# Performance work log

Hardware: AMD Instinct MI355X
Metric: run time of the kernel (lower is better)

Reference implementation:

```python
import jax, jax.numpy as jnp
import numpy as np

N = 100000   # nodes of target type
N1 = 80000   # nodes of second type
D = 128      # raw feature dim
H = 64       # hidden dim
C = 16       # n_classes
G = 3        # number of graphs (metapaths)
E = 1000000  # edges per graph
K = 20       # neighbors per node for NS branch
LP_LAYERS = 3


def setup_inputs() -> dict:
    key = jax.random.key(0)
    ks = jax.random.split(key, 24)
    f = lambda i, shape: jax.random.normal(ks[i], shape, dtype=jnp.float32)
    feats0 = f(0, (N, D))
    feats1 = f(1, (N1, D))
    W0 = f(2, (D, H)) * 0.05
    b0 = jnp.zeros((H,), jnp.float32)
    W1 = f(3, (D, H)) * 0.05
    b1 = jnp.zeros((H,), jnp.float32)
    Wp = f(4, (D, H)) * 0.05
    Wcls = f(5, (H, C)) * 0.05
    bcls = jnp.zeros((C,), jnp.float32)
    alpha = f(6, (N, 1)) * 0.1
    attention = f(7, (N, G, 1))
    y = jax.random.randint(ks[8], (N,), 0, C)
    labels_one_hot = jax.nn.one_hot(y, C, dtype=jnp.float32)
    byte_idx_train = jax.random.bernoulli(ks[9], 0.3, (N, 1))
    label_init = jnp.full((N, C), 1.0 / C, jnp.float32)
    nei_idx = jax.random.randint(ks[10], (N, K), 0, N1, dtype=jnp.int32)
    src0 = jax.random.randint(ks[11], (E,), 0, N, dtype=jnp.int32)
    dst0 = jax.random.randint(ks[12], (E,), 0, N, dtype=jnp.int32)
    src1 = jax.random.randint(ks[13], (E,), 0, N, dtype=jnp.int32)
    dst1 = jax.random.randint(ks[14], (E,), 0, N, dtype=jnp.int32)
    src2 = jax.random.randint(ks[15], (E,), 0, N, dtype=jnp.int32)
    dst2 = jax.random.randint(ks[16], (E,), 0, N, dtype=jnp.int32)
    return dict(feats0=feats0, feats1=feats1, W0=W0, b0=b0, W1=W1, b1=b1,
                Wp=Wp, Wcls=Wcls, bcls=bcls, alpha=alpha, attention=attention,
                labels_one_hot=labels_one_hot, label_init=label_init,
                byte_idx_train=byte_idx_train, nei_idx=nei_idx,
                src0=src0, dst0=dst0, src1=src1, dst1=dst1, src2=src2, dst2=dst2)


def _propagate(fp, h, src, dst, n):
    # edge attention: dot-product score of projected feats, softmax per dst
    s = jnp.sum(fp[src] * fp[dst], axis=-1) / np.sqrt(fp.shape[-1])   # [E]
    m = jax.ops.segment_max(s, dst, num_segments=n)                   # [N]
    e = jnp.exp(s - jnp.where(jnp.isfinite(m), m, 0.0)[dst])          # [E]
    denom = jax.ops.segment_sum(e, dst, num_segments=n)               # [N]
    att = e / (denom[dst] + 1e-16)                                    # [E]
    return jax.ops.segment_sum(att[:, None] * h[src], dst, num_segments=n)


def reference(feats0, feats1, W0, b0, W1, b1, Wp, Wcls, bcls, alpha, attention,
              labels_one_hot, label_init, byte_idx_train, nei_idx,
              src0, dst0, src1, dst1, src2, dst2):
    n = label_init.shape[0]
    masked = byte_idx_train.astype(jnp.float32)          # [N,1]
    masked_label = 1.0 - masked                          # (~mask).float()
    masked_onehot = labels_one_hot * masked              # clamp train labels

    fp = feats0 @ Wp                                     # shared projected feats [N,H]
    h_prime = []
    for src, dst in ((src0, dst0), (src1, dst1), (src2, dst2)):
        h = label_init
        for _ in range(LP_LAYERS):
            h = _propagate(fp, h, src, dst, n)
            h = h * masked_label + masked_onehot
        h_prime.append(h)
    x = jnp.stack(h_prime, axis=-1)                      # [N, C, G]
    att_g = jax.nn.softmax(attention, axis=1)            # [N, G, 1]
    logits_lp = jnp.matmul(x, att_g).squeeze(-1)         # [N, C]

    # NS_ec branch: per-type projection + neighbor-mean aggregation + classifier
    h0 = feats0 @ W0 + b0                                # [N, H]
    h1 = feats1 @ W1 + b1                                # [N1, H]
    z = h0 + jnp.mean(h1[nei_idx], axis=1)               # [N, H]
    logits_ns = z @ Wcls + bcls                          # [N, C]

    gate = jax.nn.sigmoid(alpha)
    logits = gate * logits_lp + jax.nn.sigmoid(-alpha) * logits_ns
    return logits, logits_lp, logits_ns
```

## Files before the change

### kernel.cpp

```cpp
#include <hip/hip_runtime.h>
#include <stdint.h>
#include <stddef.h>

__device__ __forceinline__ float bl(unsigned u){ return __uint_as_float(u << 16); }
__device__ __forceinline__ float bh(unsigned u){ return __uint_as_float(u & 0xffff0000u); }
__device__ __forceinline__ unsigned short f2bf(float f){
    unsigned u = __float_as_uint(f);
    unsigned r = (u + 0x7fffu + ((u >> 16) & 1u)) >> 16;
    return (unsigned short)r;
}
__device__ __forceinline__ void ntstore_u2(uint2* p, unsigned x, unsigned y){
    unsigned long long v = ((unsigned long long)y << 32) | (unsigned long long)x;
    __builtin_nontemporal_store(v, (unsigned long long*)p);
}
__device__ __forceinline__ float get_mask(const void* p, unsigned flags, int i){
    if((flags & 1u) == 0) return ((const int*)p)[i] ? 1.0f : 0.0f;
    if(flags & 2u)        return ((const float*)p)[i];
    return ((const unsigned char*)p)[i] ? 1.0f : 0.0f;
}

__global__ __launch_bounds__(256) void prep_kernel(
    const float* __restrict__ W0, const float* __restrict__ b0,
    const float* __restrict__ W1, const float* __restrict__ b1,
    const float* __restrict__ Wcls, const float* __restrict__ bcls,
    float* __restrict__ W0c, float* __restrict__ W1c,
    float* __restrict__ b0c, float* __restrict__ b1c,
    const unsigned char* __restrict__ mp, int n,
    const unsigned* __restrict__ li, long li_n, unsigned* __restrict__ flags)
{
    int t = threadIdx.x;
    if(blockIdx.x == 0){
        for(int i = t; i < 2048; i += 256){
            int d = i >> 4, c = i & 15;
            float s0 = 0.f, s1 = 0.f;
            for(int k = 0; k < 64; k++){
                float wc = Wcls[k*16 + c];
                s0 += W0[d*64 + k]*wc;
                s1 += W1[d*64 + k]*wc;
            }
            W0c[i] = s0; W1c[i] = s1;
        }
        if(t < 16){
            float s0 = 0.f, s1 = 0.f;
            for(int k = 0; k < 64; k++){
                float wc = Wcls[k*16 + t];
                s0 += b0[k]*wc; s1 += b1[k]*wc;
            }
            b0c[t] = s0 + bcls[t];
            b1c[t] = s1;
        }
    } else {
        long i = (long)(blockIdx.x - 1)*256 + t;
        unsigned f = 0;
        if(i < n){
            unsigned char b = mp[i];
            if((i & 3) && b) f |= 1u;
            if(b == 0x3Fu)   f |= 2u;
        }
        if(i < li_n){
            if(li[i] != li[0]) f |= 4u;
        }
        if(f) atomicOr(flags, f);
    }
}

__global__ __launch_bounds__(256) void proj_fused0(
    const float* __restrict__ X, const float* __restrict__ Wp,
    const float* __restrict__ W0c, const float* __restrict__ b0c,
    unsigned short* __restrict__ fph, float* __restrict__ h0c, int rows)
{
    __shared__ float Wl[128*64];
    __shared__ float Wcl[128*16];
    __shared__ float ftile[32*128];
    int t = threadIdx.x;
    for(int i = t; i < 2048; i += 256) ((float4*)Wl)[i]  = ((const float4*)Wp)[i];
    for(int i = t; i < 512;  i += 256) ((float4*)Wcl)[i] = ((const float4*)W0c)[i];
    int c4 = (t & 15)*4;
    int col16 = t & 15;
    int r2 = (t >> 4)*2;
    float bc = b0c[col16];
    for(long base = (long)blockIdx.x*32; base < rows; base += (long)gridDim.x*32){
        int nr = min(32, (int)(rows - base));
        __syncthreads();
        for(int i = t; i < nr*32; i += 256){
            int r = i >> 5, q = i & 31;
            ((float4*)ftile)[r*32 + q] = ((const float4*)X)[(base + r)*32 + q];
        }
        __syncthreads();
        float a00=0,a01=0,a02=0,a03=0, a10=0,a11=0,a12=0,a13=0;
        float c0 = bc, c1 = bc;
        #pragma unroll 4
        for(int k = 0; k < 128; k++){
            float4 w = *((const float4*)(Wl + k*64 + c4));
            float wc = Wcl[k*16 + col16];
            float x0 = ftile[r2*128 + k];
            float x1 = ftile[(r2+1)*128 + k];
            a00 += x0*w.x; a01 += x0*w.y; a02 += x0*w.z; a03 += x0*w.w; c0 += x0*wc;
            a10 += x1*w.x; a11 += x1*w.y; a12 += x1*w.z; a13 += x1*w.w; c1 += x1*wc;
        }
        if(r2 < nr){
            ushort4 o; o.x=f2bf(a00); o.y=f2bf(a01); o.z=f2bf(a02); o.w=f2bf(a03);
            *((ushort4*)(fph + (base + r2)*64 + c4)) = o;
            h0c[(base + r2)*16 + col16] = c0;
        }
        if(r2 + 1 < nr){
            ushort4 o; o.x=f2bf(a10); o.y=f2bf(a11); o.z=f2bf(a12); o.w=f2bf(a13);
            *((ushort4*)(fph + (base + r2 + 1)*64 + c4)) = o;
            h0c[(base + r2 + 1)*16 + col16] = c1;
        }
    }
}

__global__ __launch_bounds__(256) void proj16_count_kernel(
    const float* __restrict__ X, const float* __restrict__ Wc,
    const float* __restrict__ biasc, unsigned short* __restrict__ Y, int rows,
    int nbProj,
    const int* __restrict__ dst0, const int* __restrict__ dst1, const int* __restrict__ dst2,
    int* __restrict__ deg, int n, int eg)
{
    __shared__ float Wcl[128*16];
    __shared__ float ftile[64*128];
    int t = threadIdx.x;
    if(blockIdx.x < nbProj){
        for(int i = t; i < 512; i += 256) ((float4*)Wcl)[i] = ((const float4*)Wc)[i];
        int col = t & 15;
        int r4 = (t >> 4)*4;
        float bc = biasc[col];
        long base = (long)blockIdx.x*64;
        if(base < rows){
            int nr = min(64, (int)(rows - base));
            __syncthreads();
            for(int i = t; i < nr*32; i += 256){
                int r = i >> 5, q = i & 31;
                ((float4*)ftile)[r*32 + q] = ((const float4*)X)[(base + r)*32 + q];
            }
            __syncthreads();
            float acc0 = bc, acc1 = bc, acc2 = bc, acc3 = bc;
            #pragma unroll 4
            for(int k = 0; k < 128; k++){
                float wc = Wcl[k*16 + col];
                acc0 += ftile[(r4+0)*128 + k]*wc;
                acc1 += ftile[(r4+1)*128 + k]*wc;
                acc2 += ftile[(r4+2)*128 + k]*wc;
                acc3 += ftile[(r4+3)*128 + k]*wc;
            }
            if(r4+0 < nr) Y[(base + r4 + 0)*16 + col] = f2bf(acc0);
            if(r4+1 < nr) Y[(base + r4 + 1)*16 + col] = f2bf(acc1);
            if(r4+2 < nr) Y[(base + r4 + 2)*16 + col] = f2bf(acc2);
            if(r4+3 < nr) Y[(base + r4 + 3)*16 + col] = f2bf(acc3);
        }
    } else {
        long tid = (long)(blockIdx.x - nbProj)*256 + t;
        if(tid < 3L*eg){
            int g = (int)(tid / eg);
            int e = (int)(tid - (long)g*eg);
            const int* dp = g==0 ? dst0 : (g==1 ? dst1 : dst2);
            atomicAdd(&deg[(long)g*n + dp[e]], 1);
        }
    }
}

__global__ __launch_bounds__(256) void scanA_kernel(const int* __restrict__ deg,
                                                    int* __restrict__ incl,
                                                    int* __restrict__ bsum, int n3)
{
    __shared__ int sh[256];
    int t = threadIdx.x;
    long base = (long)blockIdx.x*1024 + t*4;
    int v0=0,v1=0,v2=0,v3=0;
    if(base   < n3) v0 = deg[base];
    if(base+1 < n3) v1 = deg[base+1];
    if(base+2 < n3) v2 = deg[base+2];
    if(base+3 < n3) v3 = deg[base+3];
    int tot = v0+v1+v2+v3;
    sh[t] = tot;
    __syncthreads();
    for(int ofs = 1; ofs < 256; ofs <<= 1){
        int add = (t >= ofs) ? sh[t-ofs] : 0;
        __syncthreads();
        sh[t] += add;
        __syncthreads();
    }
    int pre = sh[t] - tot;
    if(t == 255) bsum[blockIdx.x] = sh[255];
    int s0 = pre+v0, s1 = s0+v1, s2 = s1+v2, s3 = s2+v3;
    if(base   < n3) incl[base]   = s0;
    if(base+1 < n3) incl[base+1] = s1;
    if(base+2 < n3) incl[base+2] = s2;
    if(base+3 < n3) incl[base+3] = s3;
}

__global__ __launch_bounds__(512) void scanB_kernel(int* __restrict__ bsum, int nb)
{
    __shared__ int sh[512];
    int t = threadIdx.x;
    int v = (t < nb) ? bsum[t] : 0;
    sh[t] = v;
    __syncthreads();
    for(int ofs = 1; ofs < 512; ofs <<= 1){
        int add = (t >= ofs) ? sh[t-ofs] : 0;
        __syncthreads();
        sh[t] += add;
        __syncthreads();
    }
    if(t < nb) bsum[t] = sh[t] - v;
}

__global__ __launch_bounds__(256) void scanC_kernel(const int* __restrict__ incl,
                                                    const int* __restrict__ boff,
                                                    int* __restrict__ rowptr,
                                                    int* __restrict__ cursor, int n3)
{
    int i = blockIdx.x*blockDim.x + threadIdx.x;
    if(i >= n3) return;
    int ex = (i == 0) ? 0 : (incl[i-1] + boff[(i-1) >> 10]);
    rowptr[i] = ex;
    cursor[i] = ex;
    if(i == n3-1) rowptr[n3] = incl[i] + boff[i >> 10];
}

__global__ __launch_bounds__(256) void score_scatter_packed(
    const unsigned short* __restrict__ fph,
    const int* __restrict__ src0, const int* __restrict__ dst0,
    const int* __restrict__ src1, const int* __restrict__ dst1,
    const int* __restrict__ src2, const int* __restrict__ dst2,
    int* __restrict__ cursor, uint2* __restrict__ rec, int n, int eg)
{
    long tid = (long)blockIdx.x*blockDim.x + threadIdx.x;
    long gid = tid >> 3;
    long tot = 3L*eg;
    long e0 = gid*4;
    if(e0 >= tot) return;
    int l = threadIdx.x & 7;
    const uint4* f4 = (const uint4*)fph;

    int sv[4], dv[4], gv[4];
    bool ok[4];
    #pragma unroll
    for(int q = 0; q < 4; q++){
        long e = e0 + q;
        ok[q] = (e < tot);
        long ee = ok[q] ? e : (tot - 1);
        int g = (int)(ee / eg);
        int i = (int)(ee - (long)g*eg);
        const int* sp = g==0 ? src0 : (g==1 ? src1 : src2);
        const int* dp = g==0 ? dst0 : (g==1 ? dst1 : dst2);
        sv[q] = sp[i];
        dv[q] = dp[i];
        gv[q] = g;
    }
    uint4 A[4], B[4];
    #pragma unroll
    for(int q = 0; q < 4; q++){
        A[q] = f4[(long)sv[q]*8 + l];
        B[q] = f4[(long)dv[q]*8 + l];
    }
    float p[4];
    #pragma unroll
    for(int q = 0; q < 4; q++){
        float v;
        v  = bl(A[q].x)*bl(B[q].x) + bh(A[q].x)*bh(B[q].x);
        v += bl(A[q].y)*bl(B[q].y) + bh(A[q].y)*bh(B[q].y);
        v += bl(A[q].z)*bl(B[q].z) + bh(A[q].z)*bh(B[q].z);
        v += bl(A[q].w)*bl(B[q].w) + bh(A[q].w)*bh(B[q].w);
        p[q] = v;
    }
    #pragma unroll
    for(int q = 0; q < 4; q++){
        p[q] += __shfl_xor(p[q], 1);
        p[q] += __shfl_xor(p[q], 2);
        p[q] += __shfl_xor(p[q], 4);
    }
    if(l == 0){
        int pos[4];
        #pragma unroll
        for(int q = 0; q < 4; q++){
            if(ok[q]) pos[q] = atomicAdd(&cursor[(long)gv[q]*n + dv[q]], 1);
        }
        #pragma unroll
        for(int q = 0; q < 4; q++){
            if(ok[q]){
                float ev = __expf(fminf(p[q]*0.125f, 70.0f));
                ntstore_u2(&rec[pos[q]], (unsigned)sv[q], __float_as_uint(ev));
            }
        }
    }
}

__device__ __forceinline__ void prop_row_bf16(
    const uint2* __restrict__ rec, int beg, int end,
    const unsigned short* __restrict__ hg, int c4,
    float &a0, float &a1, float &a2, float &a3)
{
    float den = 0.f;
    a0 = a1 = a2 = a3 = 0.f;
    int j = beg;
    if((j & 1) && j < end){
        uint2 r = rec[j];
        float e = __uint_as_float(r.y);
        den += e;
        uint2 hv = *((const uint2*)(hg + (long)r.x*16 + c4));
        a0 += e*bl(hv.x); a1 += e*bh(hv.x); a2 += e*bl(hv.y); a3 += e*bh(hv.y);
        j++;
    }
    for(; j + 1 < end; j += 2){
        uint4 rr = *((const uint4*)(&rec[j]));
        float e0 = __uint_as_float(rr.y);
        float e1 = __uint_as_float(rr.w);
        den += e0 + e1;
        uint2 hv0 = *((const uint2*)(hg + (long)rr.x*16 + c4));
        uint2 hv1 = *((const uint2*)(hg + (long)rr.z*16 + c4));
        a0 += e0*bl(hv0.x) + e1*bl(hv1.x);
        a1 += e0*bh(hv0.x) + e1*bh(hv1.x);
        a2 += e0*bl(hv0.y) + e1*bl(hv1.y);
        a3 += e0*bh(hv0.y) + e1*bh(hv1.y);
    }
    if(j < end){
        uint2 r = rec[j];
        float e = __uint_as_float(r.y);
        den += e;
        uint2 hv = *((const uint2*)(hg + (long)r.x*16 + c4));
        a0 += e*bl(hv.x); a1 += e*bh(hv.x); a2 += e*bl(hv.y); a3 += e*bh(hv.y);
    }
    float inv = 1.0f/(den + 1e-16f);
    a0 *= inv; a1 *= inv; a2 *= inv; a3 *= inv;
}

template<int L1>
__global__ __launch_bounds__(256) void propagate_rec_kernel(
    const int* __restrict__ rowptr, const uint2* __restrict__ rec,
    const float* __restrict__ h_in_f32, const unsigned short* __restrict__ h_in_bf,
    unsigned short* __restrict__ h_next, const float* __restrict__ labels,
    const void* __restrict__ maskp, const unsigned* __restrict__ flags, int n)
{
    long tid = (long)blockIdx.x*blockDim.x + threadIdx.x;
    int row = (int)(tid >> 2);
    int c4 = (int)(tid & 3)*4;
    if(row >= 3*n) return;
    int g = row / n;
    int d = row - g*n;
    int beg = rowptr[row], end = rowptr[row+1];
    unsigned fl = *flags;
    float a0=0.f, a1=0.f, a2=0.f, a3=0.f;
    if(L1 && !(fl & 4u)){
        float v = (end > beg) ? h_in_f32[0] : 0.f;
        a0 = a1 = a2 = a3 = v;
    } else if(L1){
        float den = 0.f;
        for(int j = beg; j < end; j++){
            uint2 r = rec[j];
            float e = __uint_as_float(r.y);
            den += e;
            float4 hv = *((const float4*)(h_in_f32 + (long)r.x*16 + c4));
            a0 += e*hv.x; a1 += e*hv.y; a2 += e*hv.z; a3 += e*hv.w;
        }
        float inv = 1.0f/(den + 1e-16f);
        a0 *= inv; a1 *= inv; a2 *= inv; a3 *= inv;
    } else {
        prop_row_bf16(rec, beg, end, h_in_bf + (long)g*n*16, c4, a0, a1, a2, a3);
    }
    float mk = get_mask(maskp, fl, d);
    float im = 1.0f - mk;
    float4 lb = *((const float4*)(labels + (long)d*16 + c4));
    ushort4 o;
    o.x = f2bf(a0*im + lb.x*mk);
    o.y = f2bf(a1*im + lb.y*mk);
    o.z = f2bf(a2*im + lb.z*mk);
    o.w = f2bf(a3*im + lb.w*mk);
    *((ushort4*)(h_next + (long)row*16 + c4)) = o;
}

__global__ __launch_bounds__(256) void prop3_ns_kernel(
    const int* __restrict__ rowptr, const uint2* __restrict__ rec,
    const unsigned short* __restrict__ h_in_bf, const float* __restrict__ labels,
    const void* __restrict__ maskp, const unsigned* __restrict__ flags,
    const float* __restrict__ h0c, const unsigned short* __restrict__ h1c,
    const int* __restrict__ nei, const float* __restrict__ attn,
    const float* __restrict__ alpha, float* __restrict__ out, int n, int kk)
{
    long tid = (long)blockIdx.x*blockDim.x + threadIdx.x;
    int node = (int)(tid >> 2);
    int c4 = (int)(tid & 3)*4;
    if(node >= n) return;
    unsigned fl = *flags;
    float mk = get_mask(maskp, fl, node);
    float im = 1.0f - mk;
    float4 lb = *((const float4*)(labels + (long)node*16 + c4));

    float lp_[3][4];
    #pragma unroll
    for(int g = 0; g < 3; g++){
        int row = g*n + node;
        float a0, a1, a2, a3;
        prop_row_bf16(rec, rowptr[row], rowptr[row+1], h_in_bf + (long)g*n*16, c4,
                      a0, a1, a2, a3);
        lp_[g][0] = a0*im + lb.x*mk;
        lp_[g][1] = a1*im + lb.y*mk;
        lp_[g][2] = a2*im + lb.z*mk;
        lp_[g][3] = a3*im + lb.w*mk;
    }
    float t0 = attn[node*3], t1 = attn[node*3+1], t2 = attn[node*3+2];
    float mx = fmaxf(t0, fmaxf(t1, t2));
    float e0 = __expf(t0-mx), e1 = __expf(t1-mx), e2 = __expf(t2-mx);
    float inv = 1.0f/(e0+e1+e2);
    e0 *= inv; e1 *= inv; e2 *= inv;
    float lp0 = e0*lp_[0][0] + e1*lp_[1][0] + e2*lp_[2][0];
    float lp1 = e0*lp_[0][1] + e1*lp_[1][1] + e2*lp_[2][1];
    float lp2 = e0*lp_[0][2] + e1*lp_[1][2] + e2*lp_[2][2];
    float lp3 = e0*lp_[0][3] + e1*lp_[1][3] + e2*lp_[2][3];

    const int* nrow = nei + (long)node*kk;
    float s0=0.f, s1=0.f, s2=0.f, s3=0.f;
    for(int j = 0; j < kk; j++){
        int nb = nrow[j];
        uint2 hv = *((const uint2*)(h1c + (long)nb*16 + c4));
        s0 += bl(hv.x); s1 += bh(hv.x); s2 += bl(hv.y); s3 += bh(hv.y);
    }
    float invk = 1.0f/(float)kk;
    float4 h0 = *((const float4*)(h0c + (long)node*16 + c4));
    float ns0 = h0.x + s0*invk, ns1 = h0.y + s1*invk;
    float ns2 = h0.z + s2*invk, ns3 = h0.w + s3*invk;

    float al = alpha[node];
    float sg = 1.0f/(1.0f + __expf(-al));
    float isg = 1.0f - sg;
    long gs = (long)n*16;
    long idx = (long)node*16 + c4;
    float4 o0; o0.x = sg*lp0 + isg*ns0; o0.y = sg*lp1 + isg*ns1;
               o0.z = sg*lp2 + isg*ns2; o0.w = sg*lp3 + isg*ns3;
    float4 o1; o1.x = lp0; o1.y = lp1; o1.z = lp2; o1.w = lp3;
    float4 o2; o2.x = ns0; o2.y = ns1; o2.z = ns2; o2.w = ns3;
    *((float4*)(out + idx))        = o0;
    *((float4*)(out + gs + idx))   = o1;
    *((float4*)(out + 2*gs + idx)) = o2;
}

extern "C" void kernel_launch(void* const* d_in, const int* in_sizes, int n_in,
                              void* d_out, int out_size, void* d_ws, size_t ws_size,
                              hipStream_t stream)
{
    const float* feats0     = (const float*)d_in[0];
    const float* feats1     = (const float*)d_in[1];
    const float* W0         = (const float*)d_in[2];
    const float* b0         = (const float*)d_in[3];
    const float* W1         = (const float*)d_in[4];
    const float* b1         = (const float*)d_in[5];
    const float* Wp         = (const float*)d_in[6];
    const float* Wcls       = (const float*)d_in[7];
    const float* bcls       = (const float*)d_in[8];
    const float* alpha      = (const float*)d_in[9];
    const float* attn       = (const float*)d_in[10];
    const float* labels     = (const float*)d_in[11];
    const float* label_init = (const float*)d_in[12];
    const void*  maskp      = d_in[13];
    const int*   nei        = (const int*)d_in[14];
    const int*   src0       = (const int*)d_in[15];
    const int*   dst0       = (const int*)d_in[16];
    const int*   src1       = (const int*)d_in[17];
    const int*   dst1       = (const int*)d_in[18];
    const int*   src2       = (const int*)d_in[19];
    const int*   dst2       = (const int*)d_in[20];

    const int n  = in_sizes[9];
    const int n1 = in_sizes[1] / 128;
    const int eg = in_sizes[15];
    const int kk = in_sizes[14] / n;
    const int n3 = 3*n;

    char* ws = (char*)d_ws;
    size_t off = 0;
    auto alloc = [&](size_t bytes)->char*{
        char* p = ws + off; off += (bytes + 255) & ~(size_t)255; return p;
    };
    unsigned*       flags  = (unsigned*)      alloc(256);
    unsigned short* fph    = (unsigned short*)alloc((size_t)n*64*2);
    float*          h0c    = (float*)         alloc((size_t)n*16*4);
    unsigned short* h1c    = (unsigned short*)alloc((size_t)n1*16*2);
    float*          W0c    = (float*)         alloc(2048*4);
    float*          W1c    = (float*)         alloc(2048*4);
    float*          b0c    = (float*)         alloc(64);
    float*          b1c    = (float*)         alloc(64);
    int*            deg    = (int*)           alloc((size_t)n3*4);
    int*            cursor = (int*)           alloc((size_t)n3*4);
    int*            bsum   = (int*)           alloc(512*4);
    int*            rowptr = (int*)           alloc(((size_t)n3+1)*4);
    uint2*          rec    = (uint2*)         alloc((size_t)3*eg*8);
    unsigned short* hA     = (unsigned short*)alloc((size_t)n3*16*2);
    unsigned short* hB     = (unsigned short*)alloc((size_t)n3*16*2);
    int* incl = deg;

    hipMemsetAsync(flags, 0, 4, stream);
    hipMemsetAsync(deg, 0, (size_t)n3*4, stream);

    {
        long li_n = (long)n*16;
        unsigned gsz = 1 + (unsigned)((li_n + 255)/256);
        prep_kernel<<<gsz, 256, 0, stream>>>(W0, b0, W1, b1, Wcls, bcls,
                                             W0c, W1c, b0c, b1c,
                                             (const unsigned char*)maskp, n,
                                             (const unsigned*)label_init, li_n, flags);
    }

    proj_fused0<<<(n+31)/32, 256, 0, stream>>>(feats0, Wp, W0c, b0c, fph, h0c, n);
    {
        int nbProj = (n1 + 63)/64;
        long tot = 3L*eg;
        unsigned nbCount = (unsigned)((tot + 255)/256);
        proj16_count_kernel<<<nbProj + nbCount, 256, 0, stream>>>(
            feats1, W1c, b1c, h1c, n1, nbProj, dst0, dst1, dst2, deg, n, eg);
    }

    int nb = (n3 + 1023)/1024;
    scanA_kernel<<<nb, 256, 0, stream>>>(deg, incl, bsum, n3);
    scanB_kernel<<<1, 512, 0, stream>>>(bsum, nb);
    scanC_kernel<<<(n3+255)/256, 256, 0, stream>>>(incl, bsum, rowptr, cursor, n3);

    {
        long groups = (3L*eg + 3)/4;
        long tthreads = groups*8;
        score_scatter_packed<<<(unsigned)((tthreads+255)/256), 256, 0, stream>>>(
            fph, src0,dst0,src1,dst1,src2,dst2, cursor, rec, n, eg);
    }

    {
        long tot = (long)n3*4;
        unsigned gsz = (unsigned)((tot+255)/256);
        propagate_rec_kernel<1><<<gsz, 256, 0, stream>>>(
            rowptr, rec, label_init, nullptr, hA, labels, maskp, flags, n);
        propagate_rec_kernel<0><<<gsz, 256, 0, stream>>>(
            rowptr, rec, nullptr, hA, hB, labels, maskp, flags, n);
    }

    prop3_ns_kernel<<<(unsigned)(((long)n*4+255)/256), 256, 0, stream>>>(
        rowptr, rec, hB, labels, maskp, flags, h0c, h1c, nei, attn, alpha,
        (float*)d_out, n, kk);
}
```

Baseline: 485.1 us.

## Pack edge records into 32-bit words and interleave per-row gathers

Edge records shrink from 8 bytes (src index plus fp32 exp weight) to 4 bytes: a 17-bit source index plus a 15-bit reduced-precision exponent-weight, with scores clamped to [-10,10]. This halves the traffic of the scatter write and the three propagation reads. The constant-label first layer moves into scanC, the degree memset folds into prep_kernel, and the propagation kernels interleave two or three rows per thread to expose more independent gathers. The costs are lower softmax-weight precision and an index width that only fits node counts below 131072.

```diff
diff --git a/kernel.cpp b/kernel.cpp
--- a/kernel.cpp
+++ b/kernel.cpp
@@ -9,9 +9,8 @@
     unsigned r = (u + 0x7fffu + ((u >> 16) & 1u)) >> 16;
     return (unsigned short)r;
 }
-__device__ __forceinline__ void ntstore_u2(uint2* p, unsigned x, unsigned y){
-    unsigned long long v = ((unsigned long long)y << 32) | (unsigned long long)x;
-    __builtin_nontemporal_store(v, (unsigned long long*)p);
+__device__ __forceinline__ float dec15(unsigned e15){
+    return __uint_as_float((e15 + (112u << 10)) << 13);
 }
 __device__ __forceinline__ float get_mask(const void* p, unsigned flags, int i){
     if((flags & 1u) == 0) return ((const int*)p)[i] ? 1.0f : 0.0f;
@@ -26,7 +25,8 @@
     float* __restrict__ W0c, float* __restrict__ W1c,
     float* __restrict__ b0c, float* __restrict__ b1c,
     const unsigned char* __restrict__ mp, int n,
-    const unsigned* __restrict__ li, long li_n, unsigned* __restrict__ flags)
+    const unsigned* __restrict__ li, long li_n, unsigned* __restrict__ flags,
+    int* __restrict__ deg, int n3)
 {
     int t = threadIdx.x;
     if(blockIdx.x == 0){
@@ -51,6 +51,7 @@
         }
     } else {
         long i = (long)(blockIdx.x - 1)*256 + t;
+        if(i < n3) deg[i] = 0;
         unsigned f = 0;
         if(i < n){
             unsigned char b = mp[i];
@@ -206,17 +207,39 @@
     if(t < nb) bsum[t] = sh[t] - v;
 }
 
-__global__ __launch_bounds__(256) void scanC_kernel(const int* __restrict__ incl,
-                                                    const int* __restrict__ boff,
-                                                    int* __restrict__ rowptr,
-                                                    int* __restrict__ cursor, int n3)
+__global__ __launch_bounds__(256) void scanC_kernel(
+    const int* __restrict__ incl, const int* __restrict__ boff,
+    int* __restrict__ rowptr, int* __restrict__ cursor, int n3,
+    const float* __restrict__ label_init, const float* __restrict__ labels,
+    const void* __restrict__ maskp, const unsigned* __restrict__ flags,
+    unsigned short* __restrict__ hA, int n)
 {
     int i = blockIdx.x*blockDim.x + threadIdx.x;
     if(i >= n3) return;
     int ex = (i == 0) ? 0 : (incl[i-1] + boff[(i-1) >> 10]);
+    int en = incl[i] + boff[i >> 10];
     rowptr[i] = ex;
     cursor[i] = ex;
-    if(i == n3-1) rowptr[n3] = incl[i] + boff[i >> 10];
+    if(i == n3-1) rowptr[n3] = en;
+    unsigned fl = *flags;
+    if(!(fl & 4u)){
+        int g = i / n;
+        int d = i - g*n;
+        float mk = get_mask(maskp, fl, d);
+        float v = (en > ex) ? label_init[0]*(1.0f - mk) : 0.0f;
+        const float4* lb = (const float4*)(labels + (long)d*16);
+        ushort4* op = (ushort4*)(hA + (long)i*16);
+        #pragma unroll
+        for(int q = 0; q < 4; q++){
+            float4 l4 = lb[q];
+            ushort4 o;
+            o.x = f2bf(v + l4.x*mk);
+            o.y = f2bf(v + l4.y*mk);
+            o.z = f2bf(v + l4.z*mk);
+            o.w = f2bf(v + l4.w*mk);
+            op[q] = o;
+        }
+    }
 }
 
 __global__ __launch_bounds__(256) void score_scatter_packed(
@@ -224,7 +247,7 @@
     const int* __restrict__ src0, const int* __restrict__ dst0,
     const int* __restrict__ src1, const int* __restrict__ dst1,
     const int* __restrict__ src2, const int* __restrict__ dst2,
-    int* __restrict__ cursor, uint2* __restrict__ rec, int n, int eg)
+    int* __restrict__ cursor, unsigned* __restrict__ rec, int n, int eg)
 {
     long tid = (long)blockIdx.x*blockDim.x + threadIdx.x;
     long gid = tid >> 3;
@@ -280,59 +303,24 @@
         #pragma unroll
         for(int q = 0; q < 4; q++){
             if(ok[q]){
-                float ev = __expf(fminf(p[q]*0.125f, 70.0f));
-                ntstore_u2(&rec[pos[q]], (unsigned)sv[q], __float_as_uint(ev));
+                float s = fminf(fmaxf(p[q]*0.125f, -10.0f), 10.0f);
+                unsigned u = __float_as_uint(__expf(s)) + 0x1000u;
+                unsigned e15 = (u >> 13) - (112u << 10);
+                unsigned pk = (e15 << 17) | (unsigned)sv[q];
+                __builtin_nontemporal_store(pk, rec + pos[q]);
             }
         }
     }
 }
 
-__device__ __forceinline__ void prop_row_bf16(
-    const uint2* __restrict__ rec, int beg, int end,
-    const unsigned short* __restrict__ hg, int c4,
-    float &a0, float &a1, float &a2, float &a3)
-{
-    float den = 0.f;
-    a0 = a1 = a2 = a3 = 0.f;
-    int j = beg;
-    if((j & 1) && j < end){
-        uint2 r = rec[j];
-        float e = __uint_as_float(r.y);
-        den += e;
-        uint2 hv = *((const uint2*)(hg + (long)r.x*16 + c4));
-        a0 += e*bl(hv.x); a1 += e*bh(hv.x); a2 += e*bl(hv.y); a3 += e*bh(hv.y);
-        j++;
-    }
-    for(; j + 1 < end; j += 2){
-        uint4 rr = *((const uint4*)(&rec[j]));
-        float e0 = __uint_as_float(rr.y);
-        float e1 = __uint_as_float(rr.w);
-        den += e0 + e1;
-        uint2 hv0 = *((const uint2*)(hg + (long)rr.x*16 + c4));
-        uint2 hv1 = *((const uint2*)(hg + (long)rr.z*16 + c4));
-        a0 += e0*bl(hv0.x) + e1*bl(hv1.x);
-        a1 += e0*bh(hv0.x) + e1*bh(hv1.x);
-        a2 += e0*bl(hv0.y) + e1*bl(hv1.y);
-        a3 += e0*bh(hv0.y) + e1*bh(hv1.y);
-    }
-    if(j < end){
-        uint2 r = rec[j];
-        float e = __uint_as_float(r.y);
-        den += e;
-        uint2 hv = *((const uint2*)(hg + (long)r.x*16 + c4));
-        a0 += e*bl(hv.x); a1 += e*bh(hv.x); a2 += e*bl(hv.y); a3 += e*bh(hv.y);
-    }
-    float inv = 1.0f/(den + 1e-16f);
-    a0 *= inv; a1 *= inv; a2 *= inv; a3 *= inv;
-}
-
-template<int L1>
-__global__ __launch_bounds__(256) void propagate_rec_kernel(
-    const int* __restrict__ rowptr, const uint2* __restrict__ rec,
-    const float* __restrict__ h_in_f32, const unsigned short* __restrict__ h_in_bf,
-    unsigned short* __restrict__ h_next, const float* __restrict__ labels,
-    const void* __restrict__ maskp, const unsigned* __restrict__ flags, int n)
-{
+__global__ __launch_bounds__(256) void prop1_fallback_kernel(
+    const int* __restrict__ rowptr, const unsigned* __restrict__ rec,
+    const float* __restrict__ h_in_f32, unsigned short* __restrict__ h_next,
+    const float* __restrict__ labels, const void* __restrict__ maskp,
+    const unsigned* __restrict__ flags, int n)
+{
+    unsigned fl = *flags;
+    if(!(fl & 4u)) return;
     long tid = (long)blockIdx.x*blockDim.x + threadIdx.x;
     int row = (int)(tid >> 2);
     int c4 = (int)(tid & 3)*4;
@@ -340,27 +328,17 @@
     int g = row / n;
     int d = row - g*n;
     int beg = rowptr[row], end = rowptr[row+1];
-    unsigned fl = *flags;
-    float a0=0.f, a1=0.f, a2=0.f, a3=0.f;
-    if(L1 && !(fl & 4u)){
-        float v = (end > beg) ? h_in_f32[0] : 0.f;
-        a0 = a1 = a2 = a3 = v;
-    } else if(L1){
-        float den = 0.f;
-        for(int j = beg; j < end; j++){
-            uint2 r = rec[j];
-            float e = __uint_as_float(r.y);
-            den += e;
-            float4 hv = *((const float4*)(h_in_f32 + (long)r.x*16 + c4));
-            a0 += e*hv.x; a1 += e*hv.y; a2 += e*hv.z; a3 += e*hv.w;
-        }
-        float inv = 1.0f/(den + 1e-16f);
-        a0 *= inv; a1 *= inv; a2 *= inv; a3 *= inv;
-    } else {
-        prop_row_bf16(rec, beg, end, h_in_bf + (long)g*n*16, c4, a0, a1, a2, a3);
-    }
+    float a0=0.f, a1=0.f, a2=0.f, a3=0.f, den=0.f;
+    for(int j = beg; j < end; j++){
+        unsigned p = rec[j];
+        float e = dec15(p >> 17);
+        den += e;
+        float4 hv = *((const float4*)(h_in_f32 + (long)(p & 0x1FFFFu)*16 + c4));
+        a0 += e*hv.x; a1 += e*hv.y; a2 += e*hv.z; a3 += e*hv.w;
+    }
+    float inv = 1.0f/(den + 1e-16f);
     float mk = get_mask(maskp, fl, d);
-    float im = 1.0f - mk;
+    float im = (1.0f - mk)*inv;
     float4 lb = *((const float4*)(labels + (long)d*16 + c4));
     ushort4 o;
     o.x = f2bf(a0*im + lb.x*mk);
@@ -370,9 +348,68 @@
     *((ushort4*)(h_next + (long)row*16 + c4)) = o;
 }
 
+__global__ __launch_bounds__(256) void prop_mid_kernel(
+    const int* __restrict__ rowptr, const unsigned* __restrict__ rec,
+    const unsigned short* __restrict__ h_in, unsigned short* __restrict__ h_next,
+    const float* __restrict__ labels, const void* __restrict__ maskp,
+    const unsigned* __restrict__ flags, int n)
+{
+    long tid = (long)blockIdx.x*blockDim.x + threadIdx.x;
+    int pr = (int)(tid >> 2);
+    int c4 = (int)(tid & 3)*4;
+    int n3 = 3*n;
+    int r0 = pr*2, r1 = pr*2 + 1;
+    if(r0 >= n3) return;
+    int j0 = rowptr[r0], e0 = rowptr[r0+1];
+    int j1 = rowptr[r1], e1 = rowptr[r1+1];
+    const unsigned short* hg0 = h_in + (long)(r0/n)*n*16;
+    const unsigned short* hg1 = h_in + (long)(r1/n)*n*16;
+    float a00=0,a01=0,a02=0,a03=0, d0=0;
+    float a10=0,a11=0,a12=0,a13=0, d1=0;
+    while(j0 < e0 || j1 < e1){
+        if(j0 < e0){
+            unsigned p = rec[j0++];
+            float e = dec15(p >> 17); d0 += e;
+            uint2 hv = *((const uint2*)(hg0 + (long)(p & 0x1FFFFu)*16 + c4));
+            a00 += e*bl(hv.x); a01 += e*bh(hv.x); a02 += e*bl(hv.y); a03 += e*bh(hv.y);
+        }
+        if(j1 < e1){
+            unsigned p = rec[j1++];
+            float e = dec15(p >> 17); d1 += e;
+            uint2 hv = *((const uint2*)(hg1 + (long)(p & 0x1FFFFu)*16 + c4));
+            a10 += e*bl(hv.x); a11 += e*bh(hv.x); a12 += e*bl(hv.y); a13 += e*bh(hv.y);
+        }
+    }
+    unsigned fl = *flags;
+    {
+        int d = r0 % n;
+        float mk = get_mask(maskp, fl, d);
+        float im = (1.0f - mk)/(d0 + 1e-16f);
+        float4 lb = *((const float4*)(labels + (long)d*16 + c4));
+        ushort4 o;
+        o.x = f2bf(a00*im + lb.x*mk);
+        o.y = f2bf(a01*im + lb.y*mk);
+        o.z = f2bf(a02*im + lb.z*mk);
+        o.w = f2bf(a03*im + lb.w*mk);
+        *((ushort4*)(h_next + (long)r0*16 + c4)) = o;
+    }
+    {
+        int d = r1 % n;
+        float mk = get_mask(maskp, fl, d);
+        float im = (1.0f - mk)/(d1 + 1e-16f);
+        float4 lb = *((const float4*)(labels + (long)d*16 + c4));
+        ushort4 o;
+        o.x = f2bf(a10*im + lb.x*mk);
+        o.y = f2bf(a11*im + lb.y*mk);
+        o.z = f2bf(a12*im + lb.z*mk);
+        o.w = f2bf(a13*im + lb.w*mk);
+        *((ushort4*)(h_next + (long)r1*16 + c4)) = o;
+    }
+}
+
 __global__ __launch_bounds__(256) void prop3_ns_kernel(
-    const int* __restrict__ rowptr, const uint2* __restrict__ rec,
-    const unsigned short* __restrict__ h_in_bf, const float* __restrict__ labels,
+    const int* __restrict__ rowptr, const unsigned* __restrict__ rec,
+    const unsigned short* __restrict__ h_in, const float* __restrict__ labels,
     const void* __restrict__ maskp, const unsigned* __restrict__ flags,
     const float* __restrict__ h0c, const unsigned short* __restrict__ h1c,
     const int* __restrict__ nei, const float* __restrict__ attn,
@@ -382,32 +419,59 @@
     int node = (int)(tid >> 2);
     int c4 = (int)(tid & 3)*4;
     if(node >= n) return;
+    int j0 = rowptr[node],       e0_ = rowptr[node+1];
+    int j1 = rowptr[n+node],     e1_ = rowptr[n+node+1];
+    int j2 = rowptr[2*n+node],   e2_ = rowptr[2*n+node+1];
+    const unsigned short* hg0 = h_in;
+    const unsigned short* hg1 = h_in + (long)n*16;
+    const unsigned short* hg2 = h_in + (long)2*n*16;
+    float a[3][4] = {};
+    float dn0=0.f, dn1=0.f, dn2=0.f;
+    while(j0 < e0_ || j1 < e1_ || j2 < e2_){
+        if(j0 < e0_){
+            unsigned p = rec[j0++];
+            float e = dec15(p >> 17); dn0 += e;
+            uint2 hv = *((const uint2*)(hg0 + (long)(p & 0x1FFFFu)*16 + c4));
+            a[0][0] += e*bl(hv.x); a[0][1] += e*bh(hv.x);
+            a[0][2] += e*bl(hv.y); a[0][3] += e*bh(hv.y);
+        }
+        if(j1 < e1_){
+            unsigned p = rec[j1++];
+            float e = dec15(p >> 17); dn1 += e;
+            uint2 hv = *((const uint2*)(hg1 + (long)(p & 0x1FFFFu)*16 + c4));
+            a[1][0] += e*bl(hv.x); a[1][1] += e*bh(hv.x);
+            a[1][2] += e*bl(hv.y); a[1][3] += e*bh(hv.y);
+        }
+        if(j2 < e2_){
+            unsigned p = rec[j2++];
+            float e = dec15(p >> 17); dn2 += e;
+            uint2 hv = *((const uint2*)(hg2 + (long)(p & 0x1FFFFu)*16 + c4));
+            a[2][0] += e*bl(hv.x); a[2][1] += e*bh(hv.x);
+            a[2][2] += e*bl(hv.y); a[2][3] += e*bh(hv.y);
+        }
+    }
     unsigned fl = *flags;
     float mk = get_mask(maskp, fl, node);
     float im = 1.0f - mk;
     float4 lb = *((const float4*)(labels + (long)node*16 + c4));
-
-    float lp_[3][4];
-    #pragma unroll
-    for(int g = 0; g < 3; g++){
-        int row = g*n + node;
-        float a0, a1, a2, a3;
-        prop_row_bf16(rec, rowptr[row], rowptr[row+1], h_in_bf + (long)g*n*16, c4,
-                      a0, a1, a2, a3);
-        lp_[g][0] = a0*im + lb.x*mk;
-        lp_[g][1] = a1*im + lb.y*mk;
-        lp_[g][2] = a2*im + lb.z*mk;
-        lp_[g][3] = a3*im + lb.w*mk;
-    }
+    float i0 = im/(dn0 + 1e-16f), i1 = im/(dn1 + 1e-16f), i2 = im/(dn2 + 1e-16f);
+    float lpg[3][4];
+    lpg[0][0] = a[0][0]*i0 + lb.x*mk; lpg[0][1] = a[0][1]*i0 + lb.y*mk;
+    lpg[0][2] = a[0][2]*i0 + lb.z*mk; lpg[0][3] = a[0][3]*i0 + lb.w*mk;
+    lpg[1][0] = a[1][0]*i1 + lb.x*mk; lpg[1][1] = a[1][1]*i1 + lb.y*mk;
+    lpg[1][2] = a[1][2]*i1 + lb.z*mk; lpg[1][3] = a[1][3]*i1 + lb.w*mk;
+    lpg[2][0] = a[2][0]*i2 + lb.x*mk; lpg[2][1] = a[2][1]*i2 + lb.y*mk;
+    lpg[2][2] = a[2][2]*i2 + lb.z*mk; lpg[2][3] = a[2][3]*i2 + lb.w*mk;
+
     float t0 = attn[node*3], t1 = attn[node*3+1], t2 = attn[node*3+2];
     float mx = fmaxf(t0, fmaxf(t1, t2));
-    float e0 = __expf(t0-mx), e1 = __expf(t1-mx), e2 = __expf(t2-mx);
-    float inv = 1.0f/(e0+e1+e2);
-    e0 *= inv; e1 *= inv; e2 *= inv;
-    float lp0 = e0*lp_[0][0] + e1*lp_[1][0] + e2*lp_[2][0];
-    float lp1 = e0*lp_[0][1] + e1*lp_[1][1] + e2*lp_[2][1];
-    float lp2 = e0*lp_[0][2] + e1*lp_[1][2] + e2*lp_[2][2];
-    float lp3 = e0*lp_[0][3] + e1*lp_[1][3] + e2*lp_[2][3];
+    float w0 = __expf(t0-mx), w1 = __expf(t1-mx), w2 = __expf(t2-mx);
+    float winv = 1.0f/(w0+w1+w2);
+    w0 *= winv; w1 *= winv; w2 *= winv;
+    float lp0 = w0*lpg[0][0] + w1*lpg[1][0] + w2*lpg[2][0];
+    float lp1 = w0*lpg[0][1] + w1*lpg[1][1] + w2*lpg[2][1];
+    float lp2 = w0*lpg[0][2] + w1*lpg[1][2] + w2*lpg[2][2];
+    float lp3 = w0*lpg[0][3] + w1*lpg[1][3] + w2*lpg[2][3];
 
     const int* nrow = nei + (long)node*kk;
     float s0=0.f, s1=0.f, s2=0.f, s3=0.f;
@@ -484,21 +548,21 @@
     int*            cursor = (int*)           alloc((size_t)n3*4);
     int*            bsum   = (int*)           alloc(512*4);
     int*            rowptr = (int*)           alloc(((size_t)n3+1)*4);
-    uint2*          rec    = (uint2*)         alloc((size_t)3*eg*8);
+    unsigned*       rec    = (unsigned*)      alloc((size_t)3*eg*4);
     unsigned short* hA     = (unsigned short*)alloc((size_t)n3*16*2);
     unsigned short* hB     = (unsigned short*)alloc((size_t)n3*16*2);
     int* incl = deg;
 
     hipMemsetAsync(flags, 0, 4, stream);
-    hipMemsetAsync(deg, 0, (size_t)n3*4, stream);
-
+
+    long li_n = (long)n*16;
     {
-        long li_n = (long)n*16;
         unsigned gsz = 1 + (unsigned)((li_n + 255)/256);
         prep_kernel<<<gsz, 256, 0, stream>>>(W0, b0, W1, b1, Wcls, bcls,
                                              W0c, W1c, b0c, b1c,
                                              (const unsigned char*)maskp, n,
-                                             (const unsigned*)label_init, li_n, flags);
+                                             (const unsigned*)label_init, li_n, flags,
+                                             deg, n3);
     }
 
     proj_fused0<<<(n+31)/32, 256, 0, stream>>>(feats0, Wp, W0c, b0c, fph, h0c, n);
@@ -513,7 +577,9 @@
     int nb = (n3 + 1023)/1024;
     scanA_kernel<<<nb, 256, 0, stream>>>(deg, incl, bsum, n3);
     scanB_kernel<<<1, 512, 0, stream>>>(bsum, nb);
-    scanC_kernel<<<(n3+255)/256, 256, 0, stream>>>(incl, bsum, rowptr, cursor, n3);
+    scanC_kernel<<<(n3+255)/256, 256, 0, stream>>>(incl, bsum, rowptr, cursor, n3,
+                                                   label_init, labels, maskp, flags,
+                                                   hA, n);
 
     {
         long groups = (3L*eg + 3)/4;
@@ -522,14 +588,10 @@
             fph, src0,dst0,src1,dst1,src2,dst2, cursor, rec, n, eg);
     }
 
-    {
-        long tot = (long)n3*4;
-        unsigned gsz = (unsigned)((tot+255)/256);
-        propagate_rec_kernel<1><<<gsz, 256, 0, stream>>>(
-            rowptr, rec, label_init, nullptr, hA, labels, maskp, flags, n);
-        propagate_rec_kernel<0><<<gsz, 256, 0, stream>>>(
-            rowptr, rec, nullptr, hA, hB, labels, maskp, flags, n);
-    }
+    prop1_fallback_kernel<<<(unsigned)(((long)n3*4+255)/256), 256, 0, stream>>>(
+        rowptr, rec, label_init, hA, labels, maskp, flags, n);
+    prop_mid_kernel<<<(unsigned)(((long)(n3/2)*4+255)/256), 256, 0, stream>>>(
+        rowptr, rec, hA, hB, labels, maskp, flags, n);
 
     prop3_ns_kernel<<<(unsigned)(((long)n*4+255)/256), 256, 0, stream>>>(
         rowptr, rec, hB, labels, maskp, flags, h0c, h1c, nei, attn, alpha,
```

After: 534.6 us. +10.2%, slower.
